# Optimization experiments

Hardware: AMD Instinct MI355X
Metric: run time of the kernel (lower is better)

## Reference

```python
import jax, jax.numpy as jnp
import numpy as np
from math import sqrt

B, L, D_MODEL = 4, 128, 256
V, D_WORD = 50257, 768
H = 8  # n_heads; d_keys = D_MODEL // H = 32


def setup_inputs() -> dict:
    key = jax.random.key(0)
    ks = jax.random.split(key, 10)
    s = lambda k, shape, fan: jax.random.normal(k, shape, dtype=jnp.float32) / np.sqrt(fan)
    return {
        "time_series_embedding": jax.random.normal(ks[0], (B, L, D_MODEL), dtype=jnp.float32),
        "word_embedding": jax.random.normal(ks[1], (V, D_WORD), dtype=jnp.float32) * 0.02,
        "Wq": s(ks[2], (D_MODEL, D_MODEL), D_MODEL),
        "bq": jnp.zeros((D_MODEL,), jnp.float32),
        "Wk": s(ks[3], (D_WORD, D_MODEL), D_WORD),
        "bk": jnp.zeros((D_MODEL,), jnp.float32),
        "Wv": s(ks[4], (D_WORD, D_MODEL), D_WORD),
        "bv": jnp.zeros((D_MODEL,), jnp.float32),
        "Wo": s(ks[5], (D_MODEL, D_MODEL), D_MODEL),
        "bo": jnp.zeros((D_MODEL,), jnp.float32),
    }


def reference(time_series_embedding, word_embedding, Wq, bq, Wk, bk, Wv, bv, Wo, bo):
    b, l, _ = time_series_embedding.shape
    v, _ = word_embedding.shape
    h = H
    e = D_MODEL // h
    # projections
    query = (time_series_embedding @ Wq + bq).reshape(b, l, h, e)   # [B,L,H,E]
    key = (word_embedding @ Wk + bk).reshape(v, h, e)               # [V,H,E]
    value = (word_embedding @ Wv + bv).reshape(v, h, e)             # [V,H,E]
    scale = 1.0 / sqrt(e)
    # scores over full vocab: [B,H,V,L]
    scores = jnp.einsum('blhe,vhe->bhvl', query, key)
    # NOTE: faithful to source -- softmax over the LAST axis (l, the query dim)
    attn = jax.nn.softmax(scale * scores, axis=-1)
    # dropout is identity in eval mode
    reprog = jnp.einsum('bhvl,vhe->blhe', attn, value).reshape(b, l, h * e)
    return reprog @ Wo + bo  # [B,L,d_model]
```

## Files before the change

### kernel.cpp

```cpp
#include <hip/hip_runtime.h>
#include <hip/hip_bf16.h>
#include <string.h>

#define BB 4
#define LL 128
#define DM 256
#define VV 50257
#define VPAD 50304
#define DW 768
#define HH 8
#define EE 32

typedef __attribute__((ext_vector_type(8))) short sh8;
typedef __attribute__((ext_vector_type(4))) short sh4;
typedef __attribute__((ext_vector_type(4))) float f32x4;

static __device__ inline unsigned short bfbits(float x) {
  __hip_bfloat16 h = __float2bfloat16(x);
  unsigned short u;
  __builtin_memcpy(&u, &h, 2);
  return u;
}

#define GLDS16(gsrc, ldst)                                                    \
  __builtin_amdgcn_global_load_lds(                                          \
      (const __attribute__((address_space(1))) void*)(gsrc),                 \
      (__attribute__((address_space(3))) void*)(ldst), 16, 0, 0)

#define WAIT_VM(N)                                                           \
  __builtin_amdgcn_sched_barrier(0);                                         \
  asm volatile("s_waitcnt vmcnt(" #N ")" ::: "memory");                      \
  __builtin_amdgcn_sched_barrier(0)
#define WAIT_LGKM0                                                           \
  asm volatile("s_waitcnt lgkmcnt(0)" ::: "memory");                         \
  __builtin_amdgcn_sched_barrier(0)
#define SBARRIER                                                             \
  __builtin_amdgcn_sched_barrier(0);                                         \
  __builtin_amdgcn_s_barrier();                                              \
  __builtin_amdgcn_sched_barrier(0)

#if __has_builtin(__builtin_amdgcn_mfma_f32_16x16x16bf16_1k)
#define MFMA16(A, B, C) __builtin_amdgcn_mfma_f32_16x16x16bf16_1k(A, B, C, 0, 0, 0)
#elif __has_builtin(__builtin_amdgcn_mfma_f32_16x16x16_bf16)
#define MFMA16(A, B, C) __builtin_amdgcn_mfma_f32_16x16x16_bf16(A, B, C, 0, 0, 0)
#else
static __device__ inline f32x4 mfma16_asm(sh4 a, sh4 b, f32x4 c) {
  asm volatile("v_mfma_f32_16x16x16_bf16 %0, %1, %2, %0"
               : "+v"(c) : "v"(a), "v"(b));
  return c;
}
#define MFMA16(A, B, C) mfma16_asm(A, B, C)
#endif

__global__ __launch_bounds__(256) void prep_kernel(
    const float* __restrict__ Wk, const float* __restrict__ Wv,
    unsigned short* __restrict__ Wkt, unsigned short* __restrict__ Wvt,
    const float* __restrict__ tse, const float* __restrict__ Wq,
    const float* __restrict__ bq, unsigned short* __restrict__ Qb) {
  __shared__ float tileS[64][65];
  int bid = blockIdx.x;
  int t = threadIdx.x;
  if (bid < 96) {
    int z = bid / 48, rem = bid - z * 48;
    int x = rem % 12, y = rem / 12;
    const float* src = z ? Wv : Wk;
    unsigned short* dst = z ? Wvt : Wkt;
    int k0 = x * 64, n0 = y * 64;
    int c = t & 63, rb = t >> 6;
#pragma unroll
    for (int j = 0; j < 16; ++j) {
      int r = j * 4 + rb;
      tileS[r][c] = src[(size_t)(k0 + r) * DM + n0 + c];
    }
    __syncthreads();
#pragma unroll
    for (int j = 0; j < 16; ++j) {
      int r = j * 4 + rb;
      dst[(size_t)(n0 + r) * DW + k0 + c] = bfbits(tileS[c][r]);
    }
  } else {
    int r = bid - 96;
    int n = t;
    float* row = &tileS[0][0];
    row[n] = tse[r * DM + n];
    __syncthreads();
    float acc = bq[n];
#pragma unroll 8
    for (int k = 0; k < DM; ++k)
      acc = fmaf(row[k], Wq[k * DM + n], acc);
    const float scale = 0.17677669529663687f * 1.4426950408889634f;
    Qb[r * DM + n] = bfbits(acc * scale);
  }
}

__global__ __launch_bounds__(256, 2) void kvproj_kernel(
    const float* __restrict__ WE, const unsigned short* __restrict__ Wkt,
    const unsigned short* __restrict__ Wvt, const float* __restrict__ bk,
    const float* __restrict__ bv, unsigned short* __restrict__ Kbh,
    unsigned short* __restrict__ Vbt) {
  __shared__ float WEf[2][128 * 32];
  __shared__ short Kbuf[2][128 * 32];
  __shared__ short Vbuf[2][128 * 32];

  int bx = blockIdx.x;
  int v0 = (bx >> 1) * 128;
  int colbase = (bx & 1) * 128;
  int t = threadIdx.x;
  int w = t >> 6, lane = t & 63, a = lane & 15, quad = lane >> 4;
  int wm = w >> 1, wn = w & 1;

  auto stage = [&](int kt, int p) {
#pragma unroll
    for (int i = 0; i < 4; ++i) {
      int s = w * 256 + i * 64 + lane;
      int row = s >> 3;
      int cc = (s & 7) ^ (row & 7);
      int grow = v0 + row;
      if (grow > VV - 1) grow = VV - 1;
      GLDS16(WE + (size_t)grow * DW + kt * 32 + cc * 4,
             &WEf[p][(w * 256 + i * 64) * 4]);
    }
#pragma unroll
    for (int i = 0; i < 2; ++i) {
      int s = w * 128 + i * 64 + lane;
      int row = s >> 2;
      int cc = (s & 3) ^ ((row >> 1) & 3);
      GLDS16(Wkt + (size_t)(colbase + row) * DW + kt * 32 + cc * 8,
             &Kbuf[p][(w * 128 + i * 64) * 8]);
      GLDS16(Wvt + (size_t)(colbase + row) * DW + kt * 32 + cc * 8,
             &Vbuf[p][(w * 128 + i * 64) * 8]);
    }
  };

  f32x4 Ck[4][4], Cv[4][4];
#pragma unroll
  for (int mb = 0; mb < 4; ++mb)
#pragma unroll
    for (int nb = 0; nb < 4; ++nb) {
      Ck[mb][nb] = (f32x4){0.f, 0.f, 0.f, 0.f};
      Cv[mb][nb] = (f32x4){0.f, 0.f, 0.f, 0.f};
    }

  stage(0, 0);
  stage(1, 1);

  for (int kt = 0; kt < 24; ++kt) {
    int p = kt & 1;
    if (kt < 23) {
      WAIT_VM(8);
    } else {
      WAIT_VM(0);
    }
    SBARRIER;

    sh8 A[4], Bk[4], Bv[4];
#pragma unroll
    for (int mb = 0; mb < 4; ++mb) {
      int row = wm * 64 + mb * 16 + a;
      const float* rp = &WEf[p][row * 32];
      f32x4 lo = *(const f32x4*)(rp + ((2 * quad) ^ (a & 7)) * 4);
      f32x4 hi = *(const f32x4*)(rp + ((2 * quad + 1) ^ (a & 7)) * 4);
      sh4 l4 = {(short)bfbits(lo[0]), (short)bfbits(lo[1]),
                (short)bfbits(lo[2]), (short)bfbits(lo[3])};
      sh4 h4 = {(short)bfbits(hi[0]), (short)bfbits(hi[1]),
                (short)bfbits(hi[2]), (short)bfbits(hi[3])};
      A[mb] = __builtin_shufflevector(l4, h4, 0, 1, 2, 3, 4, 5, 6, 7);
    }
#pragma unroll
    for (int nb = 0; nb < 4; ++nb) {
      int krow = (wn * 4 + nb) * 16 + a;
      int cp = (quad ^ ((krow >> 1) & 3)) * 8;
      Bk[nb] = *(const sh8*)&Kbuf[p][krow * 32 + cp];
      Bv[nb] = *(const sh8*)&Vbuf[p][krow * 32 + cp];
    }
#pragma unroll
    for (int mb = 0; mb < 4; ++mb)
#pragma unroll
      for (int nb = 0; nb < 4; ++nb) {
        Ck[mb][nb] = __builtin_amdgcn_mfma_f32_16x16x32_bf16(
            A[mb], Bk[nb], Ck[mb][nb], 0, 0, 0);
        Cv[mb][nb] = __builtin_amdgcn_mfma_f32_16x16x32_bf16(
            A[mb], Bv[nb], Cv[mb][nb], 0, 0, 0);
      }

    WAIT_LGKM0;
    SBARRIER;
    if (kt < 22) stage(kt + 2, p);
  }

  float bkv[4], bvv[4];
#pragma unroll
  for (int nb = 0; nb < 4; ++nb) {
    int n = colbase + (wn * 4 + nb) * 16 + a;
    bkv[nb] = bk[n];
    bvv[nb] = bv[n];
  }
#pragma unroll
  for (int mb = 0; mb < 4; ++mb)
#pragma unroll
    for (int nb = 0; nb < 4; ++nb) {
      int m0 = v0 + wm * 64 + mb * 16 + quad * 4;
      int n = colbase + (wn * 4 + nb) * 16 + a;
      int hh = n >> 5, e = n & 31;
      sh4 vq;
#pragma unroll
      for (int r = 0; r < 4; ++r) {
        int m = m0 + r;
        bool ok = m < VV;
        Kbh[((size_t)hh * VPAD + m) * EE + e] =
            ok ? bfbits(Ck[mb][nb][r] + bkv[nb]) : 0;
        vq[r] = ok ? (short)bfbits(Cv[mb][nb][r] + bvv[nb]) : (short)0;
      }
      *(sh4*)&Vbt[(size_t)n * VPAD + m0] = vq;
    }
}

__global__ __launch_bounds__(256) void attn_kernel(
    const unsigned short* __restrict__ Qb, const unsigned short* __restrict__ Kbh,
    const unsigned short* __restrict__ Vbt, float* __restrict__ part, int bpb,
    int nc) {
  __shared__ float Cred[2][32][129];

  int bh = blockIdx.x / bpb;
  int chunk = blockIdx.x - bh * bpb;
  int b = bh >> 3, h = bh & 7;
  int t = threadIdx.x;
  int w = t >> 6;
  int lane = t & 63;
  int a = lane & 15;
  int quad = lane >> 4;

  const unsigned short* Kh = Kbh + (size_t)h * VPAD * EE;

  sh8 qf[8];
  const unsigned short* qbase = Qb + (size_t)(b * LL) * DM + h * EE;
#pragma unroll
  for (int tau = 0; tau < 8; ++tau)
    qf[tau] = *(const sh8*)(qbase + (size_t)(tau * 16 + a) * DM + quad * 8);

  f32x4 C2[2][8];
#pragma unroll
  for (int nb = 0; nb < 2; ++nb)
#pragma unroll
    for (int tau = 0; tau < 8; ++tau)
      C2[nb][tau] = (f32x4){0.f, 0.f, 0.f, 0.f};

  const int ntiles = VPAD >> 6;

  sh8 af;
  sh4 av[2];
  {
    int v0 = chunk << 6;
    af = *(const sh8*)(Kh + (size_t)(v0 + 16 * w + a) * EE + quad * 8);
#pragma unroll
    for (int nb = 0; nb < 2; ++nb)
      av[nb] = *(const sh4*)(Vbt + (size_t)(h * EE + nb * 16 + a) * VPAD +
                             v0 + 16 * w + quad * 4);
  }

  for (int tile = chunk; tile < ntiles; tile += bpb) {
    f32x4 S[8];
#pragma unroll
    for (int tau = 0; tau < 8; ++tau) {
      f32x4 z = {0.f, 0.f, 0.f, 0.f};
      S[tau] = __builtin_amdgcn_mfma_f32_16x16x32_bf16(af, qf[tau], z, 0, 0, 0);
    }

    sh8 af2 = af;
    sh4 av2[2] = {av[0], av[1]};
    int nt = tile + bpb;
    if (nt < ntiles) {
      int v0n = nt << 6;
      af2 = *(const sh8*)(Kh + (size_t)(v0n + 16 * w + a) * EE + quad * 8);
#pragma unroll
      for (int nb = 0; nb < 2; ++nb)
        av2[nb] = *(const sh4*)(Vbt + (size_t)(h * EE + nb * 16 + a) * VPAD +
                                v0n + 16 * w + quad * 4);
    }

    float sm[4], inv[4];
#pragma unroll
    for (int r = 0; r < 4; ++r) sm[r] = 0.f;
#pragma unroll
    for (int tau = 0; tau < 8; ++tau)
#pragma unroll
      for (int r = 0; r < 4; ++r) {
        float ex = __builtin_amdgcn_exp2f(S[tau][r]);
        S[tau][r] = ex;
        sm[r] += ex;
      }
#pragma unroll
    for (int msk = 1; msk <= 8; msk <<= 1)
#pragma unroll
      for (int r = 0; r < 4; ++r)
        sm[r] += __shfl_xor(sm[r], msk);
#pragma unroll
    for (int r = 0; r < 4; ++r) inv[r] = 1.f / sm[r];

    sh4 pb[8];
#pragma unroll
    for (int tau = 0; tau < 8; ++tau) {
      pb[tau][0] = (short)bfbits(S[tau][0] * inv[0]);
      pb[tau][1] = (short)bfbits(S[tau][1] * inv[1]);
      pb[tau][2] = (short)bfbits(S[tau][2] * inv[2]);
      pb[tau][3] = (short)bfbits(S[tau][3] * inv[3]);
    }

#pragma unroll
    for (int nb = 0; nb < 2; ++nb)
#pragma unroll
      for (int tau = 0; tau < 8; ++tau)
        C2[nb][tau] = MFMA16(av[nb], pb[tau], C2[nb][tau]);

    af = af2;
    av[0] = av2[0];
    av[1] = av2[1];
  }

  if (w < 2) {
#pragma unroll
    for (int nb = 0; nb < 2; ++nb)
#pragma unroll
      for (int tau = 0; tau < 8; ++tau)
#pragma unroll
        for (int r = 0; r < 4; ++r)
          Cred[w][nb * 16 + quad * 4 + r][tau * 16 + a] = C2[nb][tau][r];
  }
  __syncthreads();
  if (w >= 2) {
#pragma unroll
    for (int nb = 0; nb < 2; ++nb)
#pragma unroll
      for (int tau = 0; tau < 8; ++tau)
#pragma unroll
        for (int r = 0; r < 4; ++r)
          Cred[w - 2][nb * 16 + quad * 4 + r][tau * 16 + a] += C2[nb][tau][r];
  }
  __syncthreads();
#pragma unroll
  for (int j = 0; j < 16; ++j) {
    int f = t + 256 * j;
    int e = f & 31, l = f >> 5;
    float s = Cred[0][e][l] + Cred[1][e][l];
    size_t idx = (size_t)(b * LL + l) * DM + h * EE + e;
    if (nc > 1)
      part[(size_t)chunk * (BB * LL * DM) + idx] = s;
    else
      atomicAdd(&part[idx], s);
  }
}

__global__ __launch_bounds__(256) void outproj_kernel(
    const float* __restrict__ part, const float* __restrict__ Wo,
    const float* __restrict__ bo, float* __restrict__ out, int nc) {
  __shared__ float row[DM];
  int r = blockIdx.x, n = threadIdx.x;
  float s = 0.f;
  for (int c = 0; c < nc; ++c)
    s += part[(size_t)c * (BB * LL * DM) + (size_t)r * DM + n];
  row[n] = s;
  __syncthreads();
  float acc = bo[n];
#pragma unroll 8
  for (int k = 0; k < DM; ++k)
    acc = fmaf(row[k], Wo[k * DM + n], acc);
  out[r * DM + n] = acc;
}

extern "C" void kernel_launch(void* const* d_in, const int* in_sizes, int n_in,
                              void* d_out, int out_size, void* d_ws, size_t ws_size,
                              hipStream_t stream) {
  const float* tse = (const float*)d_in[0];
  const float* WE  = (const float*)d_in[1];
  const float* Wq  = (const float*)d_in[2];
  const float* bq  = (const float*)d_in[3];
  const float* Wk  = (const float*)d_in[4];
  const float* bk  = (const float*)d_in[5];
  const float* Wv  = (const float*)d_in[6];
  const float* bv  = (const float*)d_in[7];
  const float* Wo  = (const float*)d_in[8];
  const float* bo  = (const float*)d_in[9];
  float* out = (float*)d_out;

  char* ws = (char*)d_ws;
  const size_t QB_BYTES   = (size_t)BB * LL * DM * 2;
  const size_t KV_BYTES   = (size_t)VPAD * DM * 2;
  const size_t WT_BYTES   = (size_t)DM * DW * 2;
  const size_t PART_BYTES = (size_t)BB * LL * DM * 4;
  unsigned short* Qb  = (unsigned short*)ws;
  unsigned short* Kbh = (unsigned short*)(ws + QB_BYTES);
  unsigned short* Vbt = (unsigned short*)(ws + QB_BYTES + KV_BYTES);
  char* X = ws + QB_BYTES + 2 * KV_BYTES;
  unsigned short* Wkt = (unsigned short*)X;
  unsigned short* Wvt = (unsigned short*)(X + WT_BYTES);
  float* part = (float*)X;

  const int BPB = 32;

  const size_t NEED_PART =
      QB_BYTES + 2 * KV_BYTES + (size_t)BPB * PART_BYTES;
  const int nc = (ws_size >= NEED_PART) ? BPB : 1;

  prep_kernel<<<96 + BB * LL, 256, 0, stream>>>(Wk, Wv, Wkt, Wvt, tse, Wq, bq, Qb);
  kvproj_kernel<<<(VPAD / 128) * 2, 256, 0, stream>>>(WE, Wkt, Wvt, bk, bv, Kbh, Vbt);
  if (nc == 1)
    (void)hipMemsetAsync(part, 0, PART_BYTES, stream);
  attn_kernel<<<32 * BPB, 256, 0, stream>>>(Qb, Kbh, Vbt, part, BPB, nc);
  outproj_kernel<<<BB * LL, 256, 0, stream>>>(part, Wo, bo, out, nc);
}
```

Before: 409.4 us.

## Shrink kvproj V-tile to 64 rows and stage word embeddings as bf16 via registers

The K/V projection kernel now processes 64 vocab rows per block instead of 128, doubling the grid and raising the launch-bounds occupancy hint to 3. Word-embedding tiles are loaded into registers, converted to bf16 once and written to a swizzled LDS buffer, replacing the fp32 LDS staging and repeated per-fragment conversion. The aim is better occupancy and less LDS traffic and conversion work. The trade-off is that Wk/Wv tiles are reloaded by twice as many blocks, and the register path needs an extra LGKM wait before each barrier.

```diff
diff --git a/kernel.cpp b/kernel.cpp
--- a/kernel.cpp
+++ b/kernel.cpp
@@ -93,78 +93,86 @@
   }
 }
 
-__global__ __launch_bounds__(256, 2) void kvproj_kernel(
+__global__ __launch_bounds__(256, 3) void kvproj_kernel(
     const float* __restrict__ WE, const unsigned short* __restrict__ Wkt,
     const unsigned short* __restrict__ Wvt, const float* __restrict__ bk,
     const float* __restrict__ bv, unsigned short* __restrict__ Kbh,
     unsigned short* __restrict__ Vbt) {
-  __shared__ float WEf[2][128 * 32];
+  __shared__ short WEb[2][64 * 32];
   __shared__ short Kbuf[2][128 * 32];
   __shared__ short Vbuf[2][128 * 32];
 
   int bx = blockIdx.x;
-  int v0 = (bx >> 1) * 128;
+  int v0 = (bx >> 1) * 64;
   int colbase = (bx & 1) * 128;
   int t = threadIdx.x;
   int w = t >> 6, lane = t & 63, a = lane & 15, quad = lane >> 4;
   int wm = w >> 1, wn = w & 1;
 
-  auto stage = [&](int kt, int p) {
-#pragma unroll
-    for (int i = 0; i < 4; ++i) {
-      int s = w * 256 + i * 64 + lane;
-      int row = s >> 3;
-      int cc = (s & 7) ^ (row & 7);
-      int grow = v0 + row;
-      if (grow > VV - 1) grow = VV - 1;
-      GLDS16(WE + (size_t)grow * DW + kt * 32 + cc * 4,
-             &WEf[p][(w * 256 + i * 64) * 4]);
-    }
+  int sr = t >> 2;
+  int wc = t & 3;
+  int srow = v0 + sr;
+  if (srow > VV - 1) srow = VV - 1;
+  const float* wesrc = WE + (size_t)srow * DW + wc * 8;
+  int wphys = wc ^ ((sr >> 1) & 3);
+  const int woff = sr * 32 + (wphys << 3);
+
+  f32x4 r0, r1;
+  auto issueWE = [&](int kt) {
+    const float* p = wesrc + kt * 32;
+    r0 = *(const f32x4*)(p + 0);
+    r1 = *(const f32x4*)(p + 4);
+  };
+  auto writeWE = [&](int pb) {
+    sh4 a0 = {(short)bfbits(r0[0]), (short)bfbits(r0[1]),
+              (short)bfbits(r0[2]), (short)bfbits(r0[3])};
+    sh4 a1 = {(short)bfbits(r1[0]), (short)bfbits(r1[1]),
+              (short)bfbits(r1[2]), (short)bfbits(r1[3])};
+    *(sh8*)&WEb[pb][woff] = __builtin_shufflevector(a0, a1, 0, 1, 2, 3, 4, 5, 6, 7);
+  };
+  auto stageKV = [&](int kt, int pb) {
 #pragma unroll
     for (int i = 0; i < 2; ++i) {
       int s = w * 128 + i * 64 + lane;
       int row = s >> 2;
       int cc = (s & 3) ^ ((row >> 1) & 3);
       GLDS16(Wkt + (size_t)(colbase + row) * DW + kt * 32 + cc * 8,
-             &Kbuf[p][(w * 128 + i * 64) * 8]);
+             &Kbuf[pb][(w * 128 + i * 64) * 8]);
       GLDS16(Wvt + (size_t)(colbase + row) * DW + kt * 32 + cc * 8,
-             &Vbuf[p][(w * 128 + i * 64) * 8]);
+             &Vbuf[pb][(w * 128 + i * 64) * 8]);
     }
   };
 
-  f32x4 Ck[4][4], Cv[4][4];
-#pragma unroll
-  for (int mb = 0; mb < 4; ++mb)
+  f32x4 Ck[2][4], Cv[2][4];
+#pragma unroll
+  for (int mb = 0; mb < 2; ++mb)
 #pragma unroll
     for (int nb = 0; nb < 4; ++nb) {
       Ck[mb][nb] = (f32x4){0.f, 0.f, 0.f, 0.f};
       Cv[mb][nb] = (f32x4){0.f, 0.f, 0.f, 0.f};
     }
 
-  stage(0, 0);
-  stage(1, 1);
+  issueWE(0);
+  stageKV(0, 0);
+  writeWE(0);
+  issueWE(1);
+  stageKV(1, 1);
 
   for (int kt = 0; kt < 24; ++kt) {
     int p = kt & 1;
     if (kt < 23) {
-      WAIT_VM(8);
+      WAIT_VM(6);
     } else {
       WAIT_VM(0);
     }
+    WAIT_LGKM0;
     SBARRIER;
 
-    sh8 A[4], Bk[4], Bv[4];
-#pragma unroll
-    for (int mb = 0; mb < 4; ++mb) {
-      int row = wm * 64 + mb * 16 + a;
-      const float* rp = &WEf[p][row * 32];
-      f32x4 lo = *(const f32x4*)(rp + ((2 * quad) ^ (a & 7)) * 4);
-      f32x4 hi = *(const f32x4*)(rp + ((2 * quad + 1) ^ (a & 7)) * 4);
-      sh4 l4 = {(short)bfbits(lo[0]), (short)bfbits(lo[1]),
-                (short)bfbits(lo[2]), (short)bfbits(lo[3])};
-      sh4 h4 = {(short)bfbits(hi[0]), (short)bfbits(hi[1]),
-                (short)bfbits(hi[2]), (short)bfbits(hi[3])};
-      A[mb] = __builtin_shufflevector(l4, h4, 0, 1, 2, 3, 4, 5, 6, 7);
+    sh8 A[2], Bk[4], Bv[4];
+#pragma unroll
+    for (int mb = 0; mb < 2; ++mb) {
+      int row = wm * 32 + mb * 16 + a;
+      A[mb] = *(const sh8*)&WEb[p][row * 32 + ((quad ^ ((row >> 1) & 3)) << 3)];
     }
 #pragma unroll
     for (int nb = 0; nb < 4; ++nb) {
@@ -174,7 +182,7 @@
       Bv[nb] = *(const sh8*)&Vbuf[p][krow * 32 + cp];
     }
 #pragma unroll
-    for (int mb = 0; mb < 4; ++mb)
+    for (int mb = 0; mb < 2; ++mb)
 #pragma unroll
       for (int nb = 0; nb < 4; ++nb) {
         Ck[mb][nb] = __builtin_amdgcn_mfma_f32_16x16x32_bf16(
@@ -185,7 +193,12 @@
 
     WAIT_LGKM0;
     SBARRIER;
-    if (kt < 22) stage(kt + 2, p);
+
+    if (kt < 23) writeWE(p ^ 1);
+    if (kt < 22) {
+      issueWE(kt + 2);
+      stageKV(kt + 2, p);
+    }
   }
 
   float bkv[4], bvv[4];
@@ -196,10 +209,10 @@
     bvv[nb] = bv[n];
   }
 #pragma unroll
-  for (int mb = 0; mb < 4; ++mb)
+  for (int mb = 0; mb < 2; ++mb)
 #pragma unroll
     for (int nb = 0; nb < 4; ++nb) {
-      int m0 = v0 + wm * 64 + mb * 16 + quad * 4;
+      int m0 = v0 + wm * 32 + mb * 16 + quad * 4;
       int n = colbase + (wn * 4 + nb) * 16 + a;
       int hh = n >> 5, e = n & 31;
       sh4 vq;
@@ -402,7 +415,7 @@
   const int nc = (ws_size >= NEED_PART) ? BPB : 1;
 
   prep_kernel<<<96 + BB * LL, 256, 0, stream>>>(Wk, Wv, Wkt, Wvt, tse, Wq, bq, Qb);
-  kvproj_kernel<<<(VPAD / 128) * 2, 256, 0, stream>>>(WE, Wkt, Wvt, bk, bv, Kbh, Vbt);
+  kvproj_kernel<<<(VPAD / 64) * 2, 256, 0, stream>>>(WE, Wkt, Wvt, bk, bv, Kbh, Vbt);
   if (nc == 1)
     (void)hipMemsetAsync(part, 0, PART_BYTES, stream);
   attn_kernel<<<32 * BPB, 256, 0, stream>>>(Qb, Kbh, Vbt, part, BPB, nc);
```

Result: slower. 429.4 us (+4.9%).
